# Optimization experiments

Measured on AMD Instinct MI355X. Metric: run time of the kernel, lower is better.

The kernel has to match this reference:

```python
import jax, jax.numpy as jnp
import numpy as np
from jax import lax
import math

B, C_IN, C_OUT, D, H, W = 8, 32, 32, 16, 64, 64
K = 3            # kernel_size (cubic)
PAD = 1
E = 8            # num_experts
GROUPS = 1


def setup_inputs() -> dict:
    key = jax.random.key(0)
    k1, k2, k3, k4 = jax.random.split(key, 4)
    x = jax.random.normal(k1, (B, C_IN, D, H, W), dtype=jnp.float32)
    routing_weights = jax.random.uniform(k2, (B, E), dtype=jnp.float32)
    # kaiming_uniform_(a=sqrt(5)) equivalent bounds
    fan_in = (C_IN // GROUPS) * K * K * K
    gain = math.sqrt(2.0 / (1.0 + 5.0))
    w_bound = gain * math.sqrt(3.0 / fan_in)
    weight = jax.random.uniform(k3, (E, C_OUT, C_IN // GROUPS, K, K, K),
                                dtype=jnp.float32, minval=-w_bound, maxval=w_bound)
    b_bound = 1.0 / math.sqrt(fan_in)
    bias = jax.random.uniform(k4, (E, C_OUT), dtype=jnp.float32,
                              minval=-b_bound, maxval=b_bound)
    return {"x": x, "routing_weights": routing_weights, "weight": weight, "bias": bias}


def reference(x, routing_weights, weight, bias):
    # Faithful to the original einsum: 'bi,eocdwh->bocdwh' sums i and e
    # independently (outer-sum semantics), exactly as torch.einsum does.
    eff_kernel = jnp.einsum('bi,eocdwh->bocdwh', routing_weights, weight)  # [B,O,I/g,kd,kh,kw]
    eff_bias = jnp.einsum('bi,eo->bo', routing_weights, bias)              # [B,O]

    def conv_one(xi, ki, bi):
        # xi: [C_in,D,H,W]; ki: [O, I/g, kd,kh,kw]
        y = lax.conv_general_dilated(
            xi[None], ki,
            window_strides=(1, 1, 1),
            padding=[(PAD, PAD)] * 3,
            lhs_dilation=(1, 1, 1),
            rhs_dilation=(1, 1, 1),
            dimension_numbers=('NCDHW', 'OIDHW', 'NCDHW'),
            feature_group_count=GROUPS,
        )[0]
        return y + bi[:, None, None, None]

    return jax.vmap(conv_one)(x, eff_kernel, eff_bias)  # [B, C_OUT, D, H, W]
```

## Files before the change

kernel.cpp:

```cpp
#include <hip/hip_runtime.h>

typedef short short8 __attribute__((ext_vector_type(8)));
typedef float f32x4 __attribute__((ext_vector_type(4)));

#define XT_OFF  0u
#define WF_OFF  33554432u
#define RWB_OFF 33609728u
#define RWS_OFF 33610752u

__device__ __forceinline__ unsigned bf16rne(float f) {
    unsigned u = __float_as_uint(f);
    return (u + 0x7FFFu + ((u >> 16) & 1u)) >> 16;
}

__global__ void condconv_prep(const float* __restrict__ rw,
                              const float* __restrict__ weight,
                              const float* __restrict__ bias,
                              char* __restrict__ ws) {
    int i = blockIdx.x * 256 + threadIdx.x;
    if (i < 27648) {
        int t   = i >> 10;
        int rem = i & 1023;
        int ot  = rem >> 9;
        int l   = (rem >> 3) & 63;
        int j   = rem & 7;
        int o   = ot * 16 + (l & 15);
        int c   = 8 * (l >> 4) + j;
        float s = 0.f;
#pragma unroll
        for (int e = 0; e < 8; ++e) s += weight[((e * 32 + o) * 32 + c) * 27 + t];
        ((unsigned short*)(ws + WF_OFF))[i] = (unsigned short)bf16rne(s);
    } else if (i < 27904) {
        int k = i - 27648;
        int b = k >> 5, o = k & 31;
        float rs = 0.f, bs = 0.f;
#pragma unroll
        for (int e = 0; e < 8; ++e) { rs += rw[b * 8 + e]; bs += bias[e * 32 + o]; }
        ((float*)(ws + RWB_OFF))[k] = rs * bs;
        if (o == 0) ((float*)(ws + RWS_OFF))[b] = rs;
    }
}

__global__ __launch_bounds__(256) void condconv_cast(const float* __restrict__ x,
                                                     char* __restrict__ xT) {
    __shared__ float lds[32 * 68];
    const int tid = threadIdx.x;
    const int y = blockIdx.x, z = blockIdx.y, b = blockIdx.z;
    const float* src = x + (((size_t)(b * 32) * 16 + z) * 64 + y) * 64;
#pragma unroll
    for (int it = 0; it < 2; ++it) {
        int s = tid + it * 256;
        int c = s >> 4, xq = (s & 15) * 4;
        float4 v = *(const float4*)(src + (size_t)c * 65536 + xq);
        *(float4*)&lds[c * 68 + xq] = v;
    }
    __syncthreads();
    const int x_ = tid >> 2, cq = tid & 3;
    unsigned p[4];
#pragma unroll
    for (int jp = 0; jp < 4; ++jp) {
        float f0 = lds[(8 * cq + 2 * jp) * 68 + x_];
        float f1 = lds[(8 * cq + 2 * jp + 1) * 68 + x_];
        p[jp] = bf16rne(f0) | (bf16rne(f1) << 16);
    }
    *(uint4*)(xT + ((size_t)((b * 16 + z) * 64 + y)) * 4096 + x_ * 64 + cq * 16) =
        *(uint4*)p;
}

__global__ __launch_bounds__(256) void condconv_mfma(
        const char* __restrict__ xT,
        const char* __restrict__ wf,
        const float* __restrict__ rwbias,
        const float* __restrict__ rwsum,
        float* __restrict__ out) {
    __shared__ uint4 smem4[4752];
    char* smem = (char*)smem4;

    const int tid  = threadIdx.x;
    const int wv   = tid >> 6;
    const int lane = tid & 63;
    const int n    = lane & 15;
    const int quad = lane >> 4;
    const int y0   = blockIdx.x * 4;
    const int z    = blockIdx.y;
    const int b    = blockIdx.z;
    const int xn   = wv * 16 + n;

    if (tid < 144) {
        int row = tid >> 3, rem = tid & 7;
        int side = rem >> 2, c8 = rem & 3;
        *(uint4*)(smem + (row * 66 + side * 65) * 64 + c8 * 16) = make_uint4(0, 0, 0, 0);
    }

    const char* srcbase = xT + (size_t)b * (16 * 64 * 4096);
#pragma unroll
    for (int row = 0; row < 18; ++row) {
        const int zp = row / 6, yp = row % 6;
        const int gz = z + zp - 1, gy = y0 + yp - 1;
        uint4 v = make_uint4(0, 0, 0, 0);
        if ((unsigned)gz < 16u && (unsigned)gy < 64u)
            v = *(const uint4*)(srcbase + ((size_t)gz * 64 + gy) * 4096 + tid * 16);
        *(uint4*)(smem + (row * 66 + 1) * 64 + tid * 16) = v;
    }
    __syncthreads();

    f32x4 acc[2][4] = {};
    const char* wbase = wf + lane * 16;
    const char* base0 = smem + xn * 64 + quad * 16;

#pragma unroll
    for (int dz = 0; dz < 3; ++dz)
#pragma unroll
        for (int dy = 0; dy < 3; ++dy)
#pragma unroll
            for (int dx = 0; dx < 3; ++dx) {
                const int t = (dz * 3 + dy) * 3 + dx;
                short8 w0 = *(const short8*)(wbase + (t * 2 + 0) * 1024);
                short8 w1 = *(const short8*)(wbase + (t * 2 + 1) * 1024);
                const int off = ((dz * 6 + dy) * 66 + dx) * 64;
#pragma unroll
                for (int r = 0; r < 4; ++r) {
                    short8 xf = *(const short8*)(base0 + r * 4224 + off);
                    acc[0][r] = __builtin_amdgcn_mfma_f32_16x16x32_bf16(w0, xf, acc[0][r], 0, 0, 0);
                    acc[1][r] = __builtin_amdgcn_mfma_f32_16x16x32_bf16(w1, xf, acc[1][r], 0, 0, 0);
                }
            }

    const float rwb = rwsum[b];
#pragma unroll
    for (int ot = 0; ot < 2; ++ot)
#pragma unroll
        for (int reg = 0; reg < 4; ++reg) {
            const int o = ot * 16 + quad * 4 + reg;
            const float bb = rwbias[b * 32 + o];
            const size_t obase = ((size_t)(b * 32 + o) * 16 + z) * 64;
#pragma unroll
            for (int r = 0; r < 4; ++r)
                out[(obase + y0 + r) * 64 + xn] = rwb * acc[ot][r][reg] + bb;
        }
}

extern "C" void kernel_launch(void* const* d_in, const int* in_sizes, int n_in,
                              void* d_out, int out_size, void* d_ws, size_t ws_size,
                              hipStream_t stream) {
    const float* x      = (const float*)d_in[0];
    const float* rw     = (const float*)d_in[1];
    const float* weight = (const float*)d_in[2];
    const float* bias   = (const float*)d_in[3];
    float* out = (float*)d_out;
    char*  ws  = (char*)d_ws;

    condconv_prep<<<109, 256, 0, stream>>>(rw, weight, bias, ws);
    condconv_cast<<<dim3(64, 16, 8), 256, 0, stream>>>(x, ws + XT_OFF);
    condconv_mfma<<<dim3(16, 16, 8), 256, 0, stream>>>(
        ws + XT_OFF, ws + WF_OFF,
        (const float*)(ws + RWB_OFF), (const float*)(ws + RWS_OFF), out);
}
```

Measured before the change: 156.3 us.

## Fuse bf16 cast/transpose into conv kernel and reuse LDS row loads across dy

Removes the separate cast kernel that wrote a channel-last bf16 copy of x to workspace. The conv kernel now reads fp32 x directly, converts to bf16 and transposes into LDS. The MFMA loop is restructured so each input row fragment is loaded once and used for every dy tap. Weights for a whole dz slice are held in registers, and launch bounds request two blocks per CU. This avoids an extra global write/read of the activations and cuts redundant LDS reads, at the cost of more registers and strided fp32 global loads plus scattered 8-byte LDS stores.

```diff
diff --git a/kernel.cpp b/kernel.cpp
--- a/kernel.cpp
+++ b/kernel.cpp
@@ -1,12 +1,12 @@
 #include <hip/hip_runtime.h>
+#include <hip/hip_bf16.h>
 
 typedef short short8 __attribute__((ext_vector_type(8)));
 typedef float f32x4 __attribute__((ext_vector_type(4)));
 
-#define XT_OFF  0u
-#define WF_OFF  33554432u
-#define RWB_OFF 33609728u
-#define RWS_OFF 33610752u
+#define WF_OFF  0u
+#define RWB_OFF 55296u
+#define RWS_OFF 56320u
 
 __device__ __forceinline__ unsigned bf16rne(float f) {
     unsigned u = __float_as_uint(f);
@@ -41,34 +41,8 @@
     }
 }
 
-__global__ __launch_bounds__(256) void condconv_cast(const float* __restrict__ x,
-                                                     char* __restrict__ xT) {
-    __shared__ float lds[32 * 68];
-    const int tid = threadIdx.x;
-    const int y = blockIdx.x, z = blockIdx.y, b = blockIdx.z;
-    const float* src = x + (((size_t)(b * 32) * 16 + z) * 64 + y) * 64;
-#pragma unroll
-    for (int it = 0; it < 2; ++it) {
-        int s = tid + it * 256;
-        int c = s >> 4, xq = (s & 15) * 4;
-        float4 v = *(const float4*)(src + (size_t)c * 65536 + xq);
-        *(float4*)&lds[c * 68 + xq] = v;
-    }
-    __syncthreads();
-    const int x_ = tid >> 2, cq = tid & 3;
-    unsigned p[4];
-#pragma unroll
-    for (int jp = 0; jp < 4; ++jp) {
-        float f0 = lds[(8 * cq + 2 * jp) * 68 + x_];
-        float f1 = lds[(8 * cq + 2 * jp + 1) * 68 + x_];
-        p[jp] = bf16rne(f0) | (bf16rne(f1) << 16);
-    }
-    *(uint4*)(xT + ((size_t)((b * 16 + z) * 64 + y)) * 4096 + x_ * 64 + cq * 16) =
-        *(uint4*)p;
-}
-
-__global__ __launch_bounds__(256) void condconv_mfma(
-        const char* __restrict__ xT,
+__global__ __launch_bounds__(256, 2) void condconv_fused(
+        const float* __restrict__ x,
         const char* __restrict__ wf,
         const float* __restrict__ rwbias,
         const float* __restrict__ rwsum,
@@ -88,43 +62,72 @@
 
     if (tid < 144) {
         int row = tid >> 3, rem = tid & 7;
-        int side = rem >> 2, c8 = rem & 3;
-        *(uint4*)(smem + (row * 66 + side * 65) * 64 + c8 * 16) = make_uint4(0, 0, 0, 0);
+        int side = rem >> 2, q = rem & 3;
+        *(uint4*)(smem + (row * 66 + side * 65) * 64 + q * 16) = make_uint4(0, 0, 0, 0);
     }
 
-    const char* srcbase = xT + (size_t)b * (16 * 64 * 4096);
+    const float* xb = x + (size_t)b * (32 * 16 * 64 * 64);
 #pragma unroll
-    for (int row = 0; row < 18; ++row) {
-        const int zp = row / 6, yp = row % 6;
-        const int gz = z + zp - 1, gy = y0 + yp - 1;
-        uint4 v = make_uint4(0, 0, 0, 0);
-        if ((unsigned)gz < 16u && (unsigned)gy < 64u)
-            v = *(const uint4*)(srcbase + ((size_t)gz * 64 + gy) * 4096 + tid * 16);
-        *(uint4*)(smem + (row * 66 + 1) * 64 + tid * 16) = v;
+    for (int i = 0; i < 9; ++i) {
+        const int s   = tid + i * 256;
+        const int row = s >> 7;
+        const int rem = s & 127;
+        const int c4  = rem & 7;
+        const int x4  = rem >> 3;
+        const int zp  = row / 6, yp = row - zp * 6;
+        const int gz  = z + zp - 1, gy = y0 + yp - 1;
+        float4 v0 = {0, 0, 0, 0}, v1 = v0, v2 = v0, v3 = v0;
+        if ((unsigned)gz < 16u && (unsigned)gy < 64u) {
+            const float* p = xb + (((size_t)(4 * c4) * 16 + gz) * 64 + gy) * 64 + 4 * x4;
+            v0 = *(const float4*)(p);
+            v1 = *(const float4*)(p + 65536);
+            v2 = *(const float4*)(p + 131072);
+            v3 = *(const float4*)(p + 196608);
+        }
+        const float a0[4] = {v0.x, v0.y, v0.z, v0.w};
+        const float a1[4] = {v1.x, v1.y, v1.z, v1.w};
+        const float a2[4] = {v2.x, v2.y, v2.z, v2.w};
+        const float a3[4] = {v3.x, v3.y, v3.z, v3.w};
+#pragma unroll
+        for (int xi = 0; xi < 4; ++xi) {
+            union { __hip_bfloat162 h2[2]; uint2 u; } g;
+            g.h2[0] = __float22bfloat162_rn(make_float2(a0[xi], a1[xi]));
+            g.h2[1] = __float22bfloat162_rn(make_float2(a2[xi], a3[xi]));
+            *(uint2*)(smem + (row * 66 + 4 * x4 + xi + 1) * 64 + c4 * 8) = g.u;
+        }
     }
     __syncthreads();
 
     f32x4 acc[2][4] = {};
-    const char* wbase = wf + lane * 16;
-    const char* base0 = smem + xn * 64 + quad * 16;
+    const char* wb = wf + lane * 16;
 
 #pragma unroll
-    for (int dz = 0; dz < 3; ++dz)
+    for (int dz = 0; dz < 3; ++dz) {
+        short8 wreg[9][2];
 #pragma unroll
-        for (int dy = 0; dy < 3; ++dy)
+        for (int tt = 0; tt < 9; ++tt) {
+            wreg[tt][0] = *(const short8*)(wb + ((dz * 9 + tt) * 2 + 0) * 1024);
+            wreg[tt][1] = *(const short8*)(wb + ((dz * 9 + tt) * 2 + 1) * 1024);
+        }
+#pragma unroll
+        for (int yq = 0; yq < 6; ++yq) {
 #pragma unroll
             for (int dx = 0; dx < 3; ++dx) {
-                const int t = (dz * 3 + dy) * 3 + dx;
-                short8 w0 = *(const short8*)(wbase + (t * 2 + 0) * 1024);
-                short8 w1 = *(const short8*)(wbase + (t * 2 + 1) * 1024);
-                const int off = ((dz * 6 + dy) * 66 + dx) * 64;
+                short8 xf = *(const short8*)(
+                    smem + ((dz * 6 + yq) * 66 + xn + dx) * 64 + quad * 16);
 #pragma unroll
-                for (int r = 0; r < 4; ++r) {
-                    short8 xf = *(const short8*)(base0 + r * 4224 + off);
-                    acc[0][r] = __builtin_amdgcn_mfma_f32_16x16x32_bf16(w0, xf, acc[0][r], 0, 0, 0);
-                    acc[1][r] = __builtin_amdgcn_mfma_f32_16x16x32_bf16(w1, xf, acc[1][r], 0, 0, 0);
+                for (int dy = 0; dy < 3; ++dy) {
+                    const int r = yq - dy;
+                    if (r >= 0 && r < 4) {
+                        acc[0][r] = __builtin_amdgcn_mfma_f32_16x16x32_bf16(
+                            wreg[dy * 3 + dx][0], xf, acc[0][r], 0, 0, 0);
+                        acc[1][r] = __builtin_amdgcn_mfma_f32_16x16x32_bf16(
+                            wreg[dy * 3 + dx][1], xf, acc[1][r], 0, 0, 0);
+                    }
                 }
             }
+        }
+    }
 
     const float rwb = rwsum[b];
 #pragma unroll
@@ -151,8 +154,7 @@
     char*  ws  = (char*)d_ws;
 
     condconv_prep<<<109, 256, 0, stream>>>(rw, weight, bias, ws);
-    condconv_cast<<<dim3(64, 16, 8), 256, 0, stream>>>(x, ws + XT_OFF);
-    condconv_mfma<<<dim3(16, 16, 8), 256, 0, stream>>>(
-        ws + XT_OFF, ws + WF_OFF,
+    condconv_fused<<<dim3(16, 16, 8), 256, 0, stream>>>(
+        x, ws + WF_OFF,
         (const float*)(ws + RWB_OFF), (const float*)(ws + RWS_OFF), out);
 }
```

After: 167.0 us. 1.07x slower.
